# Kernel tuning notes

Measured on AMD Instinct MI355X. Metric: run time of the kernel, lower is better.

The kernel has to match this reference:

```python
import jax, jax.numpy as jnp
import numpy as np

TEMPERATURE = 0.07
BASE_TEMPERATURE = 0.07


def setup_inputs() -> dict:
    key = jax.random.key(0)
    k1, k2 = jax.random.split(key)
    N, D = 8192, 512
    features = jax.random.normal(k1, (N, D), dtype=jnp.float32)
    labels = jax.random.randint(k2, (N,), 0, 64, dtype=jnp.int64 if jax.config.jax_enable_x64 else jnp.int32)
    return {"features": features, "labels": labels, "rotation_multiplier": 2}


def reference(features, labels, rotation_multiplier):
    k = int(rotation_multiplier)
    N = features.shape[0]
    B = N // k
    # L2-normalize rows (torch F.normalize clamps norm at eps=1e-12)
    norm = jnp.maximum(jnp.linalg.norm(features, axis=1, keepdims=True), 1e-12)
    f = features / norm
    sim = jnp.matmul(f, f.T) / TEMPERATURE  # [N, N]

    # block positive mask: groups of k rows share a label; compare group labels
    lab = labels.reshape(B, k)[:, 0]  # [B]
    same = lab[:, None] == lab[None, :]  # [B, B]
    mask = jnp.repeat(jnp.repeat(same, k, axis=0), k, axis=1)  # [N, N]
    eye = jnp.eye(N, dtype=bool)
    mask = mask & ~eye

    # stable masked log-softmax with diagonal removed from denominator
    logits_max = jax.lax.stop_gradient(jnp.max(sim, axis=1, keepdims=True))
    logits = sim - logits_max
    exp_logits = jnp.exp(logits)
    denom = exp_logits.sum(axis=1, keepdims=True) - jnp.diagonal(exp_logits)[:, None] + 1e-8
    log_prob = logits - jnp.log(denom)

    mask_f = mask.astype(logits.dtype)
    mask_sum = mask_f.sum(axis=1)  # [N]
    valid = mask_sum > 0
    mean_log_prob_pos = (log_prob * mask_f).sum(axis=1) / jnp.maximum(mask_sum, 1.0)
    per_sample = -(TEMPERATURE / BASE_TEMPERATURE) * mean_log_prob_pos
    n_valid = valid.sum().astype(logits.dtype)
    loss = jnp.where(valid, per_sample, 0.0).sum() / jnp.maximum(n_valid, 1.0)
    return loss
```

## Files before the change

### kernel.cpp

```cpp
#include <hip/hip_runtime.h>
#include <hip/hip_bf16.h>

#define TEMP_INV 14.285714285714286f
#define FSCALE 16.0f
#define T1S (TEMP_INV / 256.0f)

typedef __attribute__((ext_vector_type(4))) float f32x4;
typedef __attribute__((ext_vector_type(4))) int i32x4;
typedef __attribute__((ext_vector_type(8))) int i32x8;

#define ASYNC_COPY16(gp, lp)                                                  \
  __builtin_amdgcn_global_load_lds(                                          \
      (__attribute__((address_space(1))) const void*)(gp),                    \
      (__attribute__((address_space(3))) void*)(lp), 16, 0, 0)

__global__ __launch_bounds__(256) void norm_k(const float* __restrict__ feat,
                                              uchar* __restrict__ fq,
                                              const int* __restrict__ labels,
                                              const int* __restrict__ kptr,
                                              int* __restrict__ glab,
                                              float* __restrict__ gacc,
                                              int* __restrict__ dcnt,
                                              int N, int D) {
  const int row = (blockIdx.x * 256 + threadIdx.x) >> 6;
  const int lane = threadIdx.x & 63;
  if (row < N) {
    const float4* fr = (const float4*)(feat + (size_t)row * D);
    float4 v0 = fr[lane * 2];
    float4 v1 = fr[lane * 2 + 1];
    float ss = v0.x * v0.x + v0.y * v0.y + v0.z * v0.z + v0.w * v0.w +
               v1.x * v1.x + v1.y * v1.y + v1.z * v1.z + v1.w * v1.w;
    #pragma unroll
    for (int off = 32; off; off >>= 1) ss += __shfl_xor(ss, off, 64);
    const float inv = FSCALE / fmaxf(sqrtf(ss), 1e-12f);
    int w0 = 0, w1 = 0;
    w0 = __builtin_amdgcn_cvt_pk_fp8_f32(v0.x * inv, v0.y * inv, w0, false);
    w0 = __builtin_amdgcn_cvt_pk_fp8_f32(v0.z * inv, v0.w * inv, w0, true);
    w1 = __builtin_amdgcn_cvt_pk_fp8_f32(v1.x * inv, v1.y * inv, w1, false);
    w1 = __builtin_amdgcn_cvt_pk_fp8_f32(v1.z * inv, v1.w * inv, w1, true);
    uint2 o; o.x = (uint)w0; o.y = (uint)w1;
    const int pofs = (lane >> 4) * 128 + (lane & 3) * 32 + ((lane >> 2) & 3) * 8;
    *(uint2*)(fq + (size_t)row * D + pofs) = o;
    if (lane == 0) {
      const int k = *kptr;
      glab[row] = labels[(size_t)(row / k) * k];
    }
  }
  if (blockIdx.x == 0 && threadIdx.x < 3) {
    if (threadIdx.x < 2) gacc[threadIdx.x] = 0.f;
    else *dcnt = 0;
  }
}

__global__ __launch_bounds__(256, 4) void gemm_k(const uchar* __restrict__ fq,
                                                 const int* __restrict__ glab,
                                                 float* __restrict__ part,
                                                 int N, int D) {
  __shared__ uchar As[128 * 128];
  __shared__ uchar Bs[128 * 128];
  const int t = threadIdx.x;
  const int lane = t & 63;
  const int wid = t >> 6;
  const int wrow = wid >> 1, wcol = wid & 1;
  const int quad = lane >> 4, l15 = lane & 15;

  const int nb = N / 128;
  const int total = nb * (nb + 1) / 2;
  int gidx = blockIdx.x;
  if ((total & 7) == 0) {
    const int per = total >> 3;
    gidx = (blockIdx.x & 7) * per + (blockIdx.x >> 3);
  }
  int idx = gidx, bi = 0;
  while (idx >= nb - bi) { idx -= nb - bi; bi++; }
  const int bj = bi + idx;
  const int i0 = bi * 128, j0 = bj * 128;
  const bool diagblk = (bi == bj);

  f32x4 acc[4][4];
  #pragma unroll
  for (int mi = 0; mi < 4; mi++)
    #pragma unroll
    for (int ni = 0; ni < 4; ni++) {
      f32x4 z = {0.f, 0.f, 0.f, 0.f};
      acc[mi][ni] = z;
    }

  uchar* sb = (wid < 2) ? As : Bs;
  const int rbase = (wid & 1) * 64;
  const int rowstart = ((wid < 2) ? i0 : j0) + rbase;
  const int lrow = lane >> 3;
  const int lch = lane & 7;

  for (int kb = 0; kb < D; kb += 128) {
    __syncthreads();
    #pragma unroll
    for (int i = 0; i < 8; i++) {
      const int rl = 8 * i + lrow;
      const int cg = lch ^ (rl & 7);
      ASYNC_COPY16(fq + (size_t)(rowstart + rl) * D + kb + cg * 16,
                   sb + (rbase + 8 * i) * 128);
    }
    __syncthreads();
    i32x8 av[4];
    #pragma unroll
    for (int mi = 0; mi < 4; mi++) {
      const int r = wrow * 64 + mi * 16 + l15;
      i32x4 lo = *(const i32x4*)&As[r * 128 + (((2 * quad) ^ (r & 7)) << 4)];
      i32x4 hi = *(const i32x4*)&As[r * 128 + (((2 * quad + 1) ^ (r & 7)) << 4)];
      av[mi] = (i32x8){lo.x, lo.y, lo.z, lo.w, hi.x, hi.y, hi.z, hi.w};
    }
    #pragma unroll
    for (int ni = 0; ni < 4; ni++) {
      const int r = wcol * 64 + ni * 16 + l15;
      i32x4 lo = *(const i32x4*)&Bs[r * 128 + (((2 * quad) ^ (r & 7)) << 4)];
      i32x4 hi = *(const i32x4*)&Bs[r * 128 + (((2 * quad + 1) ^ (r & 7)) << 4)];
      i32x8 bv = (i32x8){lo.x, lo.y, lo.z, lo.w, hi.x, hi.y, hi.z, hi.w};
      #pragma unroll
      for (int mi = 0; mi < 4; mi++)
        acc[mi][ni] = __builtin_amdgcn_mfma_scale_f32_16x16x128_f8f6f4(
            av[mi], bv, acc[mi][ni], 0, 0, 0, 127, 0, 127);
    }
  }

  __syncthreads();
  float* sf = (float*)As;
  const int colbase = j0 + wcol * 64 + l15;
  int clab[4];
  #pragma unroll
  for (int ni = 0; ni < 4; ni++) clab[ni] = glab[colbase + ni * 16];

  float colE[4] = {0.f, 0.f, 0.f, 0.f};
  float colP[4] = {0.f, 0.f, 0.f, 0.f};

  #pragma unroll
  for (int mi = 0; mi < 4; mi++) {
    const int lrw = wrow * 64 + mi * 16 + quad * 4;
    #pragma unroll
    for (int r = 0; r < 4; r++) {
      const int row = i0 + lrw + r;
      const int rlab = glab[row];
      float Ssum = 0.f, Psum = 0.f;
      #pragma unroll
      for (int ni = 0; ni < 4; ni++) {
        const int col = colbase + ni * 16;
        const float val = acc[mi][ni][r];
        const float lg = fmaf(val, T1S, -TEMP_INV);
        const bool diag = diagblk && (row == col);
        const float e = diag ? 0.f : __expf(lg);
        const float pm = (!diag && rlab == clab[ni]) ? lg : 0.f;
        Ssum += e; Psum += pm;
        colE[ni] += e; colP[ni] += pm;
      }
      #pragma unroll
      for (int off = 8; off; off >>= 1) {
        Ssum += __shfl_xor(Ssum, off, 64);
        Psum += __shfl_xor(Psum, off, 64);
      }
      if (l15 == 0) {
        sf[wcol * 128 + lrw + r]       = Ssum;
        sf[256 + wcol * 128 + lrw + r] = Psum;
      }
    }
  }
  if (!diagblk) {
    #pragma unroll
    for (int ni = 0; ni < 4; ni++) {
      float e = colE[ni];
      float p = colP[ni];
      e += __shfl_xor(e, 16, 64);
      e += __shfl_xor(e, 32, 64);
      p += __shfl_xor(p, 16, 64);
      p += __shfl_xor(p, 32, 64);
      const int lcol = wcol * 64 + ni * 16 + l15;
      if (quad == 0) {
        sf[512 + wrow * 128 + lcol] = e;
        sf[768 + wrow * 128 + lcol] = p;
      }
    }
  }
  __syncthreads();
  float* dst = part + (size_t)gidx * 512;
  if (t < 128) {
    dst[t]       = sf[t] + sf[128 + t];
    dst[128 + t] = sf[256 + t] + sf[384 + t];
  } else if (!diagblk) {
    const int u = t - 128;
    dst[256 + u] = sf[512 + u] + sf[640 + u];
    dst[384 + u] = sf[768 + u] + sf[896 + u];
  }
}

__global__ __launch_bounds__(1024) void reduce_loss_k(const float* __restrict__ part,
                                                      const int* __restrict__ glab,
                                                      const int* __restrict__ labels,
                                                      const int* __restrict__ kptr,
                                                      float* __restrict__ gacc,
                                                      int* __restrict__ dcnt,
                                                      float* __restrict__ out, int N) {
  const int nb = N / 128;
  const int b = blockIdx.x;
  const int tt = threadIdx.x;
  const int t = tt & 127;
  const int sl = tt >> 7;
  const int k = *kptr;
  const int B = N / k;

  __shared__ int h[64];
  if (tt < 64) h[tt] = 0;
  __syncthreads();
  for (int g = tt; g < B; g += 1024) {
    int lb = labels[(size_t)g * k];
    if (lb >= 0 && lb < 64) atomicAdd(&h[lb], 1);
  }

  float S = 0.f, P = 0.f;
  const int base = b * nb - b * (b - 1) / 2;
  for (int bj = b + sl; bj < nb; bj += 8) {
    const float* p = part + (size_t)(base + bj - b) * 512;
    S += p[t];
    P += p[128 + t];
  }
  for (int bi = sl; bi < b; bi += 8) {
    const int idx = bi * nb - bi * (bi - 1) / 2 + (b - bi);
    const float* p = part + (size_t)idx * 512;
    S += p[256 + t];
    P += p[384 + t];
  }
  __shared__ float sS[8][128], sP[8][128];
  sS[sl][t] = S; sP[sl][t] = P;
  __syncthreads();
  float l = 0.f, v = 0.f;
  if (sl == 0) {
    S = 0.f; P = 0.f;
    #pragma unroll
    for (int s = 0; s < 8; s++) { S += sS[s][t]; P += sP[s][t]; }
    const int np = h[glab[b * 128 + t]] * k - 1;
    if (np > 0) {
      l = -(P - (float)np * logf(S + 1e-8f)) / (float)np;
      v = 1.f;
    }
  }
  #pragma unroll
  for (int off = 32; off; off >>= 1) {
    l += __shfl_xor(l, off, 64);
    v += __shfl_xor(v, off, 64);
  }
  __shared__ float sl16[16], sv16[16];
  if ((tt & 63) == 0) { sl16[tt >> 6] = l; sv16[tt >> 6] = v; }
  __syncthreads();
  if (tt == 0) {
    float L = 0.f, V = 0.f;
    #pragma unroll
    for (int i = 0; i < 16; i++) { L += sl16[i]; V += sv16[i]; }
    atomicAdd(&gacc[0], L);
    atomicAdd(&gacc[1], V);
    __threadfence();
    const int prev = atomicAdd(dcnt, 1);
    if (prev == (int)gridDim.x - 1) {
      const float Lf = atomicAdd(&gacc[0], 0.f);
      const float Vf = atomicAdd(&gacc[1], 0.f);
      out[0] = Lf / fmaxf(Vf, 1.f);
    }
  }
}

extern "C" void kernel_launch(void* const* d_in, const int* in_sizes, int n_in,
                              void* d_out, int out_size, void* d_ws, size_t ws_size,
                              hipStream_t stream) {
  const float* feat = (const float*)d_in[0];
  const int* labels = (const int*)d_in[1];
  const int* kptr   = (const int*)d_in[2];
  const int N = in_sizes[1];
  const int D = in_sizes[0] / N;

  const int nb = N / 128;
  const int total = nb * (nb + 1) / 2;

  char* ws = (char*)d_ws;
  uchar* fq = (uchar*)ws;
  size_t off = (size_t)N * D;
  float* part = (float*)(ws + off); off += (size_t)total * 512 * sizeof(float);
  int* glab   = (int*)(ws + off);   off += (size_t)N * sizeof(int);
  float* gacc = (float*)(ws + off); off += 2 * sizeof(float);
  int* dcnt   = (int*)(ws + off);   off += sizeof(int);

  norm_k<<<(N + 3) / 4, 256, 0, stream>>>(feat, fq, labels, kptr, glab,
                                          gacc, dcnt, N, D);
  gemm_k<<<total, 256, 0, stream>>>(fq, glab, part, N, D);
  reduce_loss_k<<<nb, 1024, 0, stream>>>(part, glab, labels, kptr, gacc, dcnt,
                                         (float*)d_out, N);
}
```

Baseline: 129.3 us.

## Process two tiles per GEMM block and prefetch the next tile during the epilogue

Each GEMM block now handles two consecutive upper-triangle 128x128 tiles instead of one, with half as many blocks launched. The first k-slice of the second tile is loaded asynchronously while the softmax epilogue of the first tile runs, and a separate LDS buffer for the reduction scratch makes that overlap possible. This targets load latency at tile boundaries and per-block launch overhead. In exchange it uses more LDS per block, which may lower occupancy, and it halves the grid size, which can cause tail imbalance.

```diff
diff --git a/kernel.cpp b/kernel.cpp
--- a/kernel.cpp
+++ b/kernel.cpp
@@ -58,6 +58,7 @@
                                                  int N, int D) {
   __shared__ uchar As[128 * 128];
   __shared__ uchar Bs[128 * 128];
+  __shared__ float sf[1024];
   const int t = threadIdx.x;
   const int lane = t & 63;
   const int wid = t >> 6;
@@ -66,128 +67,156 @@
 
   const int nb = N / 128;
   const int total = nb * (nb + 1) / 2;
-  int gidx = blockIdx.x;
-  if ((total & 7) == 0) {
-    const int per = total >> 3;
-    gidx = (blockIdx.x & 7) * per + (blockIdx.x >> 3);
+  int gidx;
+  if ((total & 15) == 0) {
+    const int perx = total >> 4;
+    gidx = ((blockIdx.x & 7) * perx + (blockIdx.x >> 3)) * 2;
+  } else {
+    gidx = blockIdx.x * 2;
   }
   int idx = gidx, bi = 0;
   while (idx >= nb - bi) { idx -= nb - bi; bi++; }
-  const int bj = bi + idx;
-  const int i0 = bi * 128, j0 = bj * 128;
-  const bool diagblk = (bi == bj);
-
-  f32x4 acc[4][4];
-  #pragma unroll
-  for (int mi = 0; mi < 4; mi++)
-    #pragma unroll
-    for (int ni = 0; ni < 4; ni++) {
-      f32x4 z = {0.f, 0.f, 0.f, 0.f};
-      acc[mi][ni] = z;
-    }
-
+  int bj = bi + idx;
+  int i0 = bi * 128, j0 = bj * 128;
+
+  const int lrow = lane >> 3;
+  const int lch = lane & 7;
   uchar* sb = (wid < 2) ? As : Bs;
   const int rbase = (wid & 1) * 64;
-  const int rowstart = ((wid < 2) ? i0 : j0) + rbase;
-  const int lrow = lane >> 3;
-  const int lch = lane & 7;
-
-  for (int kb = 0; kb < D; kb += 128) {
+
+  #define ISSUE_DMA(ri0, rj0, kb)                                             \
+    {                                                                         \
+      const int rowstart = ((wid < 2) ? (ri0) : (rj0)) + rbase;               \
+      _Pragma("unroll")                                                       \
+      for (int i8 = 0; i8 < 8; i8++) {                                        \
+        const int rl = 8 * i8 + lrow;                                         \
+        const int cg = lch ^ (rl & 7);                                        \
+        ASYNC_COPY16(fq + (size_t)(rowstart + rl) * D + (kb) + cg * 16,       \
+                     sb + (rbase + 8 * i8) * 128);                            \
+      }                                                                       \
+    }
+
+  ISSUE_DMA(i0, j0, 0)
+  __syncthreads();
+
+  for (int tt = 0; tt < 2; tt++) {
+    const bool diagblk = (bi == bj);
+    const bool valid = (gidx < total);
+
+    f32x4 acc[4][4];
+    #pragma unroll
+    for (int mi = 0; mi < 4; mi++)
+      #pragma unroll
+      for (int ni = 0; ni < 4; ni++) {
+        f32x4 z = {0.f, 0.f, 0.f, 0.f};
+        acc[mi][ni] = z;
+      }
+
+    for (int it = 0; it < 4; it++) {
+      i32x8 av[4];
+      #pragma unroll
+      for (int mi = 0; mi < 4; mi++) {
+        const int r = wrow * 64 + mi * 16 + l15;
+        i32x4 lo = *(const i32x4*)&As[r * 128 + (((2 * quad) ^ (r & 7)) << 4)];
+        i32x4 hi = *(const i32x4*)&As[r * 128 + (((2 * quad + 1) ^ (r & 7)) << 4)];
+        av[mi] = (i32x8){lo.x, lo.y, lo.z, lo.w, hi.x, hi.y, hi.z, hi.w};
+      }
+      #pragma unroll
+      for (int ni = 0; ni < 4; ni++) {
+        const int r = wcol * 64 + ni * 16 + l15;
+        i32x4 lo = *(const i32x4*)&Bs[r * 128 + (((2 * quad) ^ (r & 7)) << 4)];
+        i32x4 hi = *(const i32x4*)&Bs[r * 128 + (((2 * quad + 1) ^ (r & 7)) << 4)];
+        i32x8 bv = (i32x8){lo.x, lo.y, lo.z, lo.w, hi.x, hi.y, hi.z, hi.w};
+        #pragma unroll
+        for (int mi = 0; mi < 4; mi++)
+          acc[mi][ni] = __builtin_amdgcn_mfma_scale_f32_16x16x128_f8f6f4(
+              av[mi], bv, acc[mi][ni], 0, 0, 0, 127, 0, 127);
+      }
+      __syncthreads();
+      if (it < 3) {
+        ISSUE_DMA(i0, j0, (it + 1) * 128)
+        __syncthreads();
+      }
+    }
+
+    const int e_i0 = i0, e_j0 = j0, e_gidx = gidx;
+    const bool e_diag = diagblk, e_valid = valid;
+    gidx++;
+    if (tt == 0) {
+      if (++bj >= nb) { bi++; bj = bi; }
+      i0 = bi * 128; j0 = bj * 128;
+      if (gidx < total) ISSUE_DMA(i0, j0, 0)
+    }
+
+    if (e_valid) {
+      const int colbase = e_j0 + wcol * 64 + l15;
+      int clab[4];
+      #pragma unroll
+      for (int ni = 0; ni < 4; ni++) clab[ni] = glab[colbase + ni * 16];
+
+      float colE[4] = {0.f, 0.f, 0.f, 0.f};
+      float colP[4] = {0.f, 0.f, 0.f, 0.f};
+
+      #pragma unroll
+      for (int mi = 0; mi < 4; mi++) {
+        const int lrw = wrow * 64 + mi * 16 + quad * 4;
+        #pragma unroll
+        for (int r = 0; r < 4; r++) {
+          const int row = e_i0 + lrw + r;
+          const int rlab = glab[row];
+          float Ssum = 0.f, Psum = 0.f;
+          #pragma unroll
+          for (int ni = 0; ni < 4; ni++) {
+            const int col = colbase + ni * 16;
+            const float val = acc[mi][ni][r];
+            const float lg = fmaf(val, T1S, -TEMP_INV);
+            const bool diag = e_diag && (row == col);
+            const float e = diag ? 0.f : __expf(lg);
+            const float pm = (!diag && rlab == clab[ni]) ? lg : 0.f;
+            Ssum += e; Psum += pm;
+            colE[ni] += e; colP[ni] += pm;
+          }
+          #pragma unroll
+          for (int off = 8; off; off >>= 1) {
+            Ssum += __shfl_xor(Ssum, off, 64);
+            Psum += __shfl_xor(Psum, off, 64);
+          }
+          if (l15 == 0) {
+            sf[wcol * 128 + lrw + r]       = Ssum;
+            sf[256 + wcol * 128 + lrw + r] = Psum;
+          }
+        }
+      }
+      if (!e_diag) {
+        #pragma unroll
+        for (int ni = 0; ni < 4; ni++) {
+          float e = colE[ni];
+          float p = colP[ni];
+          e += __shfl_xor(e, 16, 64);
+          e += __shfl_xor(e, 32, 64);
+          p += __shfl_xor(p, 16, 64);
+          p += __shfl_xor(p, 32, 64);
+          const int lcol = wcol * 64 + ni * 16 + l15;
+          if (quad == 0) {
+            sf[512 + wrow * 128 + lcol] = e;
+            sf[768 + wrow * 128 + lcol] = p;
+          }
+        }
+      }
+    }
     __syncthreads();
-    #pragma unroll
-    for (int i = 0; i < 8; i++) {
-      const int rl = 8 * i + lrow;
-      const int cg = lch ^ (rl & 7);
-      ASYNC_COPY16(fq + (size_t)(rowstart + rl) * D + kb + cg * 16,
-                   sb + (rbase + 8 * i) * 128);
+    if (e_valid) {
+      float* dst = part + (size_t)e_gidx * 512;
+      if (t < 128) {
+        dst[t]       = sf[t] + sf[128 + t];
+        dst[128 + t] = sf[256 + t] + sf[384 + t];
+      } else if (!e_diag) {
+        const int u = t - 128;
+        dst[256 + u] = sf[512 + u] + sf[640 + u];
+        dst[384 + u] = sf[768 + u] + sf[896 + u];
+      }
     }
     __syncthreads();
-    i32x8 av[4];
-    #pragma unroll
-    for (int mi = 0; mi < 4; mi++) {
-      const int r = wrow * 64 + mi * 16 + l15;
-      i32x4 lo = *(const i32x4*)&As[r * 128 + (((2 * quad) ^ (r & 7)) << 4)];
-      i32x4 hi = *(const i32x4*)&As[r * 128 + (((2 * quad + 1) ^ (r & 7)) << 4)];
-      av[mi] = (i32x8){lo.x, lo.y, lo.z, lo.w, hi.x, hi.y, hi.z, hi.w};
-    }
-    #pragma unroll
-    for (int ni = 0; ni < 4; ni++) {
-      const int r = wcol * 64 + ni * 16 + l15;
-      i32x4 lo = *(const i32x4*)&Bs[r * 128 + (((2 * quad) ^ (r & 7)) << 4)];
-      i32x4 hi = *(const i32x4*)&Bs[r * 128 + (((2 * quad + 1) ^ (r & 7)) << 4)];
-      i32x8 bv = (i32x8){lo.x, lo.y, lo.z, lo.w, hi.x, hi.y, hi.z, hi.w};
-      #pragma unroll
-      for (int mi = 0; mi < 4; mi++)
-        acc[mi][ni] = __builtin_amdgcn_mfma_scale_f32_16x16x128_f8f6f4(
-            av[mi], bv, acc[mi][ni], 0, 0, 0, 127, 0, 127);
-    }
-  }
-
-  __syncthreads();
-  float* sf = (float*)As;
-  const int colbase = j0 + wcol * 64 + l15;
-  int clab[4];
-  #pragma unroll
-  for (int ni = 0; ni < 4; ni++) clab[ni] = glab[colbase + ni * 16];
-
-  float colE[4] = {0.f, 0.f, 0.f, 0.f};
-  float colP[4] = {0.f, 0.f, 0.f, 0.f};
-
-  #pragma unroll
-  for (int mi = 0; mi < 4; mi++) {
-    const int lrw = wrow * 64 + mi * 16 + quad * 4;
-    #pragma unroll
-    for (int r = 0; r < 4; r++) {
-      const int row = i0 + lrw + r;
-      const int rlab = glab[row];
-      float Ssum = 0.f, Psum = 0.f;
-      #pragma unroll
-      for (int ni = 0; ni < 4; ni++) {
-        const int col = colbase + ni * 16;
-        const float val = acc[mi][ni][r];
-        const float lg = fmaf(val, T1S, -TEMP_INV);
-        const bool diag = diagblk && (row == col);
-        const float e = diag ? 0.f : __expf(lg);
-        const float pm = (!diag && rlab == clab[ni]) ? lg : 0.f;
-        Ssum += e; Psum += pm;
-        colE[ni] += e; colP[ni] += pm;
-      }
-      #pragma unroll
-      for (int off = 8; off; off >>= 1) {
-        Ssum += __shfl_xor(Ssum, off, 64);
-        Psum += __shfl_xor(Psum, off, 64);
-      }
-      if (l15 == 0) {
-        sf[wcol * 128 + lrw + r]       = Ssum;
-        sf[256 + wcol * 128 + lrw + r] = Psum;
-      }
-    }
-  }
-  if (!diagblk) {
-    #pragma unroll
-    for (int ni = 0; ni < 4; ni++) {
-      float e = colE[ni];
-      float p = colP[ni];
-      e += __shfl_xor(e, 16, 64);
-      e += __shfl_xor(e, 32, 64);
-      p += __shfl_xor(p, 16, 64);
-      p += __shfl_xor(p, 32, 64);
-      const int lcol = wcol * 64 + ni * 16 + l15;
-      if (quad == 0) {
-        sf[512 + wrow * 128 + lcol] = e;
-        sf[768 + wrow * 128 + lcol] = p;
-      }
-    }
-  }
-  __syncthreads();
-  float* dst = part + (size_t)gidx * 512;
-  if (t < 128) {
-    dst[t]       = sf[t] + sf[128 + t];
-    dst[128 + t] = sf[256 + t] + sf[384 + t];
-  } else if (!diagblk) {
-    const int u = t - 128;
-    dst[256 + u] = sf[512 + u] + sf[640 + u];
-    dst[384 + u] = sf[768 + u] + sf[896 + u];
   }
 }
 
@@ -276,6 +305,7 @@
 
   const int nb = N / 128;
   const int total = nb * (nb + 1) / 2;
+  const int npairs = (total + 1) / 2;
 
   char* ws = (char*)d_ws;
   uchar* fq = (uchar*)ws;
@@ -287,7 +317,7 @@
 
   norm_k<<<(N + 3) / 4, 256, 0, stream>>>(feat, fq, labels, kptr, glab,
                                           gacc, dcnt, N, D);
-  gemm_k<<<total, 256, 0, stream>>>(fq, glab, part, N, D);
+  gemm_k<<<npairs, 256, 0, stream>>>(fq, glab, part, N, D);
   reduce_loss_k<<<nb, 1024, 0, stream>>>(part, glab, labels, kptr, gacc, dcnt,
                                          (float*)d_out, N);
 }
```

After: 460.5 us. +256.2%, slower.
